# Kernel tuning notes

Measured on AMD Instinct MI355X. Metric: run time of the kernel, lower is better.

Reference implementation:

```python
import jax, jax.numpy as jnp
import numpy as np

N_NODES = 50000
N_EDGES = 600000
IN_DIM = 128
HID = 256
OUT = 3


def setup_inputs() -> dict:
    key = jax.random.key(0)
    ks = jax.random.split(key, 10)
    x = jax.random.normal(ks[0], (N_NODES, IN_DIM), dtype=jnp.float32)
    edge_index = jax.random.randint(ks[1], (2, N_EDGES), 0, N_NODES, dtype=jnp.int64)
    s = lambda k, shp: jax.random.normal(k, shp, dtype=jnp.float32) * (1.0 / np.sqrt(shp[0]))
    return {
        "x": x,
        "edge_index": edge_index,
        # SAGEConv1: lin_l (applied to aggregated neighbors, with bias), lin_r (root, no bias)
        "W1l": s(ks[2], (IN_DIM, HID)), "b1": jnp.zeros((HID,), jnp.float32), "W1r": s(ks[3], (IN_DIM, HID)),
        # SAGEConv2
        "W2l": s(ks[4], (HID, HID)), "b2": jnp.zeros((HID,), jnp.float32), "W2r": s(ks[5], (HID, HID)),
        # classification head
        "Wh": s(ks[6], (HID, OUT)), "bh": jnp.zeros((OUT,), jnp.float32),
    }


def _sage_conv(x, edge_index, Wl, b, Wr):
    """PyG SAGEConv with mean aggregation: out = lin_l(mean_{j->i} x_j) + lin_r(x_i)."""
    src, dst = edge_index[0], edge_index[1]
    n = x.shape[0]
    # gather source features and scatter-mean onto targets
    msg_sum = jax.ops.segment_sum(x[src], dst, num_segments=n)          # [N, d]
    deg = jax.ops.segment_sum(jnp.ones((src.shape[0],), x.dtype), dst, num_segments=n)
    mean = msg_sum / jnp.maximum(deg, 1.0)[:, None]                      # isolated nodes -> 0
    return mean @ Wl + b + x @ Wr


def reference(x, edge_index, W1l, b1, W1r, W2l, b2, W2r, Wh, bh):
    h = jax.nn.relu(_sage_conv(x, edge_index, W1l, b1, W1r))
    # dropout(p=0.2) is identity in eval mode
    h = jax.nn.relu(_sage_conv(h, edge_index, W2l, b2, W2r))
    return h @ Wh + bh
```

## Files before the change

kernel.cpp:

```cpp
#include <hip/hip_runtime.h>
#include <hip/hip_bf16.h>

#define N_NODES 50000
#define N_EDGES 600000
#define IN_DIM 128
#define HID 256
#define OUT_DIM 3

#define M_PAD 50048

#define SCAN_B 256
#define SCAN_NB ((N_NODES + SCAN_B - 1) / SCAN_B)

#define XQ_SCALE (255.0f / 12.0f)
#define XQ_INV   (12.0f / 255.0f)
#define XQ_OFF   (-6.0f)
#define HQ_SCALE (255.0f / 8.0f)
#define HQ_INV   (8.0f / 255.0f)

typedef __bf16 bf16x8 __attribute__((ext_vector_type(8)));
typedef float f32x4 __attribute__((ext_vector_type(4)));

static __device__ __forceinline__ unsigned short f2b(float f) {
    union { float f; unsigned u; } u; u.f = f;
    unsigned r = u.u + 0x7fffu + ((u.u >> 16) & 1u);
    return (unsigned short)(r >> 16);
}
static __device__ __forceinline__ float b2f(unsigned short b) {
    union { unsigned u; float f; } u; u.u = ((unsigned)b) << 16;
    return u.f;
}


#define SETUP_CAST (N_NODES * IN_DIM / 4)
#define SETUP_T1 (SETUP_CAST + 196608)
#define SETUP_T2 (SETUP_T1 + N_NODES * 3)
#define SETUP_TOT (SETUP_T2 + N_EDGES)

__global__ __launch_bounds__(256) void setup_kernel(
    const float* __restrict__ x, unsigned short* __restrict__ xb, unsigned* __restrict__ xq,
    const float* __restrict__ W1l, const float* __restrict__ W1r,
    const float* __restrict__ W2l, const float* __restrict__ W2r,
    unsigned short* __restrict__ W1lt, unsigned short* __restrict__ W1rt,
    unsigned short* __restrict__ W2lt, unsigned short* __restrict__ W2rt,
    const float* __restrict__ bh, float* __restrict__ out,
    const int* __restrict__ dst, int* __restrict__ counts) {
    int i = blockIdx.x * blockDim.x + threadIdx.x;
    if (i < SETUP_CAST) {
        float4 v = ((const float4*)x)[i];
        ushort4 o;
        o.x = f2b(v.x); o.y = f2b(v.y); o.z = f2b(v.z); o.w = f2b(v.w);
        ((ushort4*)xb)[i] = o;
        float t0 = fminf(fmaxf((v.x - XQ_OFF) * XQ_SCALE, 0.f), 255.f);
        float t1 = fminf(fmaxf((v.y - XQ_OFF) * XQ_SCALE, 0.f), 255.f);
        float t2 = fminf(fmaxf((v.z - XQ_OFF) * XQ_SCALE, 0.f), 255.f);
        float t3 = fminf(fmaxf((v.w - XQ_OFF) * XQ_SCALE, 0.f), 255.f);
        unsigned q = (unsigned)(t0 + 0.5f) | ((unsigned)(t1 + 0.5f) << 8) |
                     ((unsigned)(t2 + 0.5f) << 16) | ((unsigned)(t3 + 0.5f) << 24);
        xq[i] = q;
    } else if (i < SETUP_T1) {
        int j = i - SETUP_CAST;
        const float* in; unsigned short* ow; int K;
        if (j < 32768)       { in = W1l; ow = W1lt; K = IN_DIM; }
        else if (j < 65536)  { in = W1r; ow = W1rt; K = IN_DIM; j -= 32768; }
        else if (j < 131072) { in = W2l; ow = W2lt; K = HID;    j -= 65536; }
        else                 { in = W2r; ow = W2rt; K = HID;    j -= 131072; }
        int k = j >> 8;
        int n = j & 255;
        ow[(size_t)n * K + k] = f2b(in[j]);
    } else if (i < SETUP_T2) {
        int j = i - SETUP_T1;
        out[j] = bh[j % 3];
    } else if (i < SETUP_TOT) {
        int e = i - SETUP_T2;
        atomicAdd(&counts[dst[e]], 1);
    }
}


__global__ __launch_bounds__(256) void block_sum_kernel(const int* __restrict__ counts,
                                                        int* __restrict__ partial) {
    int node = blockIdx.x * SCAN_B + threadIdx.x;
    int v = (node < N_NODES) ? counts[node] : 0;
#pragma unroll
    for (int off = 32; off > 0; off >>= 1) v += __shfl_down(v, off);
    __shared__ int ws[4];
    if ((threadIdx.x & 63) == 0) ws[threadIdx.x >> 6] = v;
    __syncthreads();
    if (threadIdx.x == 0) partial[blockIdx.x] = ws[0] + ws[1] + ws[2] + ws[3];
}

__global__ __launch_bounds__(256) void scan_partial_kernel(int* __restrict__ partial) {
    __shared__ int s[SCAN_B];
    int t = threadIdx.x;
    int v = (t < SCAN_NB) ? partial[t] : 0;
    s[t] = v;
    __syncthreads();
    for (int off = 1; off < SCAN_B; off <<= 1) {
        int u = (t >= off) ? s[t - off] : 0;
        __syncthreads();
        s[t] += u;
        __syncthreads();
    }
    if (t < SCAN_NB) partial[t] = s[t] - v;
}

__global__ __launch_bounds__(256) void write_rowptr_kernel(const int* __restrict__ counts,
                                                           const int* __restrict__ partial,
                                                           int* __restrict__ row_ptr) {
    __shared__ int s[SCAN_B];
    int t = threadIdx.x;
    int node = blockIdx.x * SCAN_B + t;
    int v = (node < N_NODES) ? counts[node] : 0;
    s[t] = v;
    __syncthreads();
    for (int off = 1; off < SCAN_B; off <<= 1) {
        int u = (t >= off) ? s[t - off] : 0;
        __syncthreads();
        s[t] += u;
        __syncthreads();
    }
    if (node < N_NODES) row_ptr[node] = partial[blockIdx.x] + s[t] - v;
    if (node == 0) row_ptr[N_NODES] = N_EDGES;
}

__global__ void fill_csr_kernel(const int* __restrict__ src, const int* __restrict__ dst,
                                const int* __restrict__ row_ptr, int* __restrict__ cursor,
                                int* __restrict__ csr_src) {
    int e = blockIdx.x * blockDim.x + threadIdx.x;
    if (e < N_EDGES) {
        int d = dst[e];
        int pos = atomicAdd(&cursor[d], 1);
        csr_src[row_ptr[d] + pos] = src[e];
    }
}


__global__ __launch_bounds__(256) void cast_h1_u8_kernel(const unsigned short* __restrict__ h1,
                                                         unsigned char* __restrict__ h1q) {
    int i = blockIdx.x * blockDim.x + threadIdx.x;
    if (i >= N_NODES * HID / 8) return;
    uint4 v = ((const uint4*)h1)[i];
    unsigned w[4] = {v.x, v.y, v.z, v.w};
    unsigned b0 = 0, b1 = 0;
#pragma unroll
    for (int k = 0; k < 4; k++) {
        float f0 = b2f((unsigned short)(w[k] & 0xffff));
        float f1 = b2f((unsigned short)(w[k] >> 16));
        unsigned q0 = (unsigned)(fminf(f0 * HQ_SCALE, 255.f) + 0.5f);
        unsigned q1 = (unsigned)(fminf(f1 * HQ_SCALE, 255.f) + 0.5f);
        if (k < 2) b0 |= (q0 << (k * 16)) | (q1 << (k * 16 + 8));
        else       b1 |= (q0 << ((k - 2) * 16)) | (q1 << ((k - 2) * 16 + 8));
    }
    ((uint2*)h1q)[i] = make_uint2(b0, b1);
}


static __device__ __forceinline__ void addb(unsigned* acc, uint4 v) {
    acc[0]  += v.x & 0xff; acc[1]  += (v.x >> 8) & 0xff; acc[2]  += (v.x >> 16) & 0xff; acc[3]  += v.x >> 24;
    acc[4]  += v.y & 0xff; acc[5]  += (v.y >> 8) & 0xff; acc[6]  += (v.y >> 16) & 0xff; acc[7]  += v.y >> 24;
    acc[8]  += v.z & 0xff; acc[9]  += (v.z >> 8) & 0xff; acc[10] += (v.z >> 16) & 0xff; acc[11] += v.z >> 24;
    acc[12] += v.w & 0xff; acc[13] += (v.w >> 8) & 0xff; acc[14] += (v.w >> 16) & 0xff; acc[15] += v.w >> 24;
}

static __device__ __forceinline__ uint4 pack8(const float* a) {
    uint4 pk;
    pk.x = (unsigned)f2b(a[0]) | ((unsigned)f2b(a[1]) << 16);
    pk.y = (unsigned)f2b(a[2]) | ((unsigned)f2b(a[3]) << 16);
    pk.z = (unsigned)f2b(a[4]) | ((unsigned)f2b(a[5]) << 16);
    pk.w = (unsigned)f2b(a[6]) | ((unsigned)f2b(a[7]) << 16);
    return pk;
}

__global__ __launch_bounds__(256) void agg_mean256_u8_kernel(const unsigned char* __restrict__ featq,
                                                             const int* __restrict__ row_ptr,
                                                             const int* __restrict__ csr_src,
                                                             unsigned short* __restrict__ out) {
    int node = blockIdx.x * 4 + (threadIdx.x >> 6);
    if (node >= N_NODES) return;
    int lane = threadIdx.x & 63;
    int g = lane >> 4, lq = lane & 15;
    const uint4* f = (const uint4*)featq;
    unsigned acc[16];
#pragma unroll
    for (int j = 0; j < 16; j++) acc[j] = 0u;
    int beg = row_ptr[node], end = row_ptr[node + 1];
    int i = beg;
    for (; i + 16 <= end; i += 16) {
        int s0 = csr_src[i + g];
        int s1 = csr_src[i + 4 + g];
        int s2 = csr_src[i + 8 + g];
        int s3 = csr_src[i + 12 + g];
        uint4 v0 = f[(size_t)s0 * 16 + lq];
        uint4 v1 = f[(size_t)s1 * 16 + lq];
        uint4 v2 = f[(size_t)s2 * 16 + lq];
        uint4 v3 = f[(size_t)s3 * 16 + lq];
        addb(acc, v0); addb(acc, v1); addb(acc, v2); addb(acc, v3);
    }
    int r = end - i;
    int rem = r & 3;
    int tb = i + (r & ~3);
    bool tl = g < rem;
    uint4 u0, u1, u2, ut;
    if (r >= 4)  { int s = csr_src[i + g];     u0 = f[(size_t)s * 16 + lq]; }
    if (r >= 8)  { int s = csr_src[i + 4 + g]; u1 = f[(size_t)s * 16 + lq]; }
    if (r >= 12) { int s = csr_src[i + 8 + g]; u2 = f[(size_t)s * 16 + lq]; }
    if (tl)      { int s = csr_src[tb + g];    ut = f[(size_t)s * 16 + lq]; }
    if (r >= 4)  addb(acc, u0);
    if (r >= 8)  addb(acc, u1);
    if (r >= 12) addb(acc, u2);
    if (tl) addb(acc, ut);
#pragma unroll
    for (int j = 0; j < 16; j++) {
        acc[j] += (unsigned)__shfl_xor((int)acc[j], 32);
        acc[j] += (unsigned)__shfl_xor((int)acc[j], 16);
    }
    float inv = (end > beg) ? HQ_INV / (float)(end - beg) : 0.0f;
    if (g == 0) {
        float m[16];
#pragma unroll
        for (int j = 0; j < 16; j++) m[j] = (float)acc[j] * inv;
        uint4* orow = (uint4*)(out + (size_t)node * 256);
        orow[lq * 2]     = pack8(m);
        orow[lq * 2 + 1] = pack8(m + 8);
    }
}

__global__ __launch_bounds__(256) void agg_mean128_u8_kernel(const unsigned char* __restrict__ featq,
                                                             const int* __restrict__ row_ptr,
                                                             const int* __restrict__ csr_src,
                                                             unsigned short* __restrict__ out) {
    int node = blockIdx.x * 4 + (threadIdx.x >> 6);
    if (node >= N_NODES) return;
    int lane = threadIdx.x & 63;
    int g = lane >> 3, lq = lane & 7;
    const uint4* f = (const uint4*)featq;
    unsigned acc[16];
#pragma unroll
    for (int j = 0; j < 16; j++) acc[j] = 0u;
    int beg = row_ptr[node], end = row_ptr[node + 1];
    int i = beg;
    for (; i + 16 <= end; i += 16) {
        int s0 = csr_src[i + g];
        int s1 = csr_src[i + 8 + g];
        uint4 v0 = f[(size_t)s0 * 8 + lq];
        uint4 v1 = f[(size_t)s1 * 8 + lq];
        addb(acc, v0); addb(acc, v1);
    }
    int r = end - i;
    int rem = r & 7;
    int tb = i + (r & ~7);
    bool tl = g < rem;
    uint4 u0, ut;
    if (r >= 8) { int s = csr_src[i + g];  u0 = f[(size_t)s * 8 + lq]; }
    if (tl)     { int s = csr_src[tb + g]; ut = f[(size_t)s * 8 + lq]; }
    if (r >= 8) addb(acc, u0);
    if (tl) addb(acc, ut);
#pragma unroll
    for (int j = 0; j < 16; j++) {
        acc[j] += (unsigned)__shfl_xor((int)acc[j], 32);
        acc[j] += (unsigned)__shfl_xor((int)acc[j], 16);
        acc[j] += (unsigned)__shfl_xor((int)acc[j], 8);
    }
    bool has = end > beg;
    float inv = has ? XQ_INV / (float)(end - beg) : 0.0f;
    float o = has ? XQ_OFF : 0.0f;
    if (g == 0) {
        float m[16];
#pragma unroll
        for (int j = 0; j < 16; j++) m[j] = (float)acc[j] * inv + o;
        uint4* orow = (uint4*)(out + (size_t)node * 128);
        orow[lq * 2]     = pack8(m);
        orow[lq * 2 + 1] = pack8(m + 8);
    }
}


template <int KP>
static __device__ __forceinline__ void gemm_pipe_loop(
    const unsigned short* __restrict__ A0, const unsigned short* __restrict__ W0t,
    const unsigned short* __restrict__ A1, const unsigned short* __restrict__ W1t,
    unsigned short* As, unsigned short* Bs,
    int m0, int n0, int t, int w, int quad, int lr, f32x4 (&acc)[2][8]) {
    constexpr int KI = KP / 32;
    constexpr int NIT = 2 * KI;
    const int kb = t & 3;
    const int r  = t >> 2;

    const unsigned short* Aa[2] = {A0, A1};
    const unsigned short* Wa[2] = {W0t, W1t};

    uint4 ra0, ra1, rb0, rb1;
    auto gload = [&](int it) {
        int p = it / KI;
        int k0 = (it % KI) * 32 + kb * 8;
        const unsigned short* A = Aa[p];
        const unsigned short* Wt = Wa[p];
        ra0 = *(const uint4*)(A + (size_t)(m0 + r) * KP + k0);
        ra1 = *(const uint4*)(A + (size_t)(m0 + 64 + r) * KP + k0);
        rb0 = *(const uint4*)(Wt + (size_t)(n0 + r) * KP + k0);
        rb1 = *(const uint4*)(Wt + (size_t)(n0 + 64 + r) * KP + k0);
    };
    auto wlds = [&](int buf) {
        unsigned short* pa = As + buf * 4096;
        unsigned short* pb = Bs + buf * 4096;
        *(uint4*)&pa[(kb * 128 + r) * 8] = ra0;
        *(uint4*)&pa[(kb * 128 + 64 + r) * 8] = ra1;
        *(uint4*)&pb[(kb * 128 + r) * 8] = rb0;
        *(uint4*)&pb[(kb * 128 + 64 + r) * 8] = rb1;
    };

    gload(0);
    wlds(0);
    __syncthreads();
    for (int it = 0; it < NIT; ++it) {
        if (it + 1 < NIT) gload(it + 1);
        const unsigned short* pa = As + (it & 1) * 4096;
        const unsigned short* pb = Bs + (it & 1) * 4096;
        bf16x8 a[2], b[8];
        a[0] = *(const bf16x8*)&pa[(quad * 128 + w * 32 + lr) * 8];
        a[1] = *(const bf16x8*)&pa[(quad * 128 + w * 32 + 16 + lr) * 8];
#pragma unroll
        for (int nt = 0; nt < 8; nt++)
            b[nt] = *(const bf16x8*)&pb[(quad * 128 + nt * 16 + lr) * 8];
#pragma unroll
        for (int mt = 0; mt < 2; mt++)
#pragma unroll
            for (int nt = 0; nt < 8; nt++)
                acc[mt][nt] = __builtin_amdgcn_mfma_f32_16x16x32_bf16(a[mt], b[nt], acc[mt][nt], 0, 0, 0);
        if (it + 1 < NIT) {
            wlds((it + 1) & 1);
            __syncthreads();
        }
    }
}

template <int KP>
__global__ __launch_bounds__(256) void gemm_pipe_kernel(
    const unsigned short* __restrict__ A0, const unsigned short* __restrict__ W0t,
    const unsigned short* __restrict__ A1, const unsigned short* __restrict__ W1t,
    const float* __restrict__ bias, unsigned short* __restrict__ out, int M) {
    __shared__ __align__(16) unsigned short As[2 * 4096];
    __shared__ __align__(16) unsigned short Bs[2 * 4096];

    const int t = threadIdx.x;
    const int w = t >> 6, l = t & 63;
    const int quad = l >> 4, lr = l & 15;
    const int m0 = blockIdx.y * 128, n0 = blockIdx.x * 128;

    f32x4 acc[2][8];
    const f32x4 zero = {0.f, 0.f, 0.f, 0.f};
#pragma unroll
    for (int mt = 0; mt < 2; mt++)
#pragma unroll
        for (int nt = 0; nt < 8; nt++) acc[mt][nt] = zero;

    float bias_r[8];
#pragma unroll
    for (int nt = 0; nt < 8; nt++) bias_r[nt] = bias[n0 + nt * 16 + lr];

    gemm_pipe_loop<KP>(A0, W0t, A1, W1t, As, Bs, m0, n0, t, w, quad, lr, acc);

#pragma unroll
    for (int mt = 0; mt < 2; mt++)
#pragma unroll
        for (int r = 0; r < 4; r++) {
            int gm = m0 + w * 32 + mt * 16 + quad * 4 + r;
            if (gm >= M) continue;
            unsigned short* orow = out + (size_t)gm * HID;
#pragma unroll
            for (int nt = 0; nt < 8; nt++) {
                float v = fmaxf(acc[mt][nt][r] + bias_r[nt], 0.f);
                orow[n0 + nt * 16 + lr] = f2b(v);
            }
        }
}

template <int KP>
__global__ __launch_bounds__(256) void gemm_pipe_head_kernel(
    const unsigned short* __restrict__ A0, const unsigned short* __restrict__ W0t,
    const unsigned short* __restrict__ A1, const unsigned short* __restrict__ W1t,
    const float* __restrict__ bias, const float* __restrict__ Wh,
    float* __restrict__ out, int M) {
    __shared__ __align__(16) unsigned short As[2 * 4096];
    __shared__ __align__(16) unsigned short Bs[2 * 4096];

    const int t = threadIdx.x;
    const int w = t >> 6, l = t & 63;
    const int quad = l >> 4, lr = l & 15;
    const int m0 = blockIdx.y * 128, n0 = blockIdx.x * 128;

    f32x4 acc[2][8];
    const f32x4 zero = {0.f, 0.f, 0.f, 0.f};
#pragma unroll
    for (int mt = 0; mt < 2; mt++)
#pragma unroll
        for (int nt = 0; nt < 8; nt++) acc[mt][nt] = zero;

    float bias_r[8];
    float wh_r[8][3];
#pragma unroll
    for (int nt = 0; nt < 8; nt++) {
        int gn = n0 + nt * 16 + lr;
        bias_r[nt] = bias[gn];
        wh_r[nt][0] = Wh[gn * 3 + 0];
        wh_r[nt][1] = Wh[gn * 3 + 1];
        wh_r[nt][2] = Wh[gn * 3 + 2];
    }

    gemm_pipe_loop<KP>(A0, W0t, A1, W1t, As, Bs, m0, n0, t, w, quad, lr, acc);

#pragma unroll
    for (int mt = 0; mt < 2; mt++)
#pragma unroll
        for (int r = 0; r < 4; r++) {
            int gm = m0 + w * 32 + mt * 16 + quad * 4 + r;
            float p0 = 0.f, p1 = 0.f, p2 = 0.f;
#pragma unroll
            for (int nt = 0; nt < 8; nt++) {
                float v = fmaxf(acc[mt][nt][r] + bias_r[nt], 0.f);
                p0 += v * wh_r[nt][0];
                p1 += v * wh_r[nt][1];
                p2 += v * wh_r[nt][2];
            }
#pragma unroll
            for (int off = 1; off < 16; off <<= 1) {
                p0 += __shfl_xor(p0, off);
                p1 += __shfl_xor(p1, off);
                p2 += __shfl_xor(p2, off);
            }
            if (lr == 0 && gm < M) {
                atomicAdd(&out[(size_t)gm * 3 + 0], p0);
                atomicAdd(&out[(size_t)gm * 3 + 1], p1);
                atomicAdd(&out[(size_t)gm * 3 + 2], p2);
            }
        }
}


extern "C" void kernel_launch(void* const* d_in, const int* in_sizes, int n_in,
                              void* d_out, int out_size, void* d_ws, size_t ws_size,
                              hipStream_t stream) {
    const float* x   = (const float*)d_in[0];
    const int*   ei  = (const int*)d_in[1];
    const int*   src = ei;
    const int*   dst = ei + N_EDGES;
    const float* W1l = (const float*)d_in[2];
    const float* b1  = (const float*)d_in[3];
    const float* W1r = (const float*)d_in[4];
    const float* W2l = (const float*)d_in[5];
    const float* b2  = (const float*)d_in[6];
    const float* W2r = (const float*)d_in[7];
    const float* Wh  = (const float*)d_in[8];
    const float* bh  = (const float*)d_in[9];
    float* out = (float*)d_out;

    char* ws = (char*)d_ws;
    size_t off = 0;
    auto alloc = [&](size_t bytes) -> void* {
        void* p = ws + off;
        off = (off + bytes + 255) & ~(size_t)255;
        return p;
    };
    int* counts   = (int*)alloc((size_t)N_NODES * 4);
    int* row_ptr  = (int*)alloc((size_t)(N_NODES + 1) * 4);
    int* cursor   = (int*)alloc((size_t)N_NODES * 4);
    int* partial  = (int*)alloc((size_t)SCAN_NB * 4);
    int* csr_src  = (int*)alloc((size_t)N_EDGES * 4);
    unsigned short* xb   = (unsigned short*)alloc((size_t)M_PAD * IN_DIM * 2);
    unsigned short* agg  = (unsigned short*)alloc((size_t)M_PAD * HID * 2);
    unsigned short* h1   = (unsigned short*)alloc((size_t)M_PAD * HID * 2);
    unsigned short* W1lt = (unsigned short*)alloc((size_t)IN_DIM * HID * 2);
    unsigned short* W1rt = (unsigned short*)alloc((size_t)IN_DIM * HID * 2);
    unsigned short* W2lt = (unsigned short*)alloc((size_t)HID * HID * 2);
    unsigned short* W2rt = (unsigned short*)alloc((size_t)HID * HID * 2);
    unsigned*       xq   = (unsigned*)alloc((size_t)N_NODES * IN_DIM);
    unsigned char*  h1q  = (unsigned char*)alloc((size_t)N_NODES * HID);

    hipMemsetAsync(counts, 0, (size_t)N_NODES * 4, stream);
    hipMemsetAsync(cursor, 0, (size_t)N_NODES * 4, stream);

    setup_kernel<<<(SETUP_TOT + 255) / 256, 256, 0, stream>>>(
        x, xb, xq, W1l, W1r, W2l, W2r, W1lt, W1rt, W2lt, W2rt, bh, out, dst, counts);

    const int eblocks = (N_EDGES + 255) / 256;
    block_sum_kernel<<<SCAN_NB, SCAN_B, 0, stream>>>(counts, partial);
    scan_partial_kernel<<<1, SCAN_B, 0, stream>>>(partial);
    write_rowptr_kernel<<<SCAN_NB, SCAN_B, 0, stream>>>(counts, partial, row_ptr);
    fill_csr_kernel<<<eblocks, 256, 0, stream>>>(src, dst, row_ptr, cursor, csr_src);

    const int nblocks4 = (N_NODES + 3) / 4;
    dim3 gg(HID / 128, M_PAD / 128);

    agg_mean128_u8_kernel<<<nblocks4, 256, 0, stream>>>((const unsigned char*)xq, row_ptr, csr_src, agg);
    gemm_pipe_kernel<IN_DIM><<<gg, 256, 0, stream>>>(agg, W1lt, xb, W1rt, b1, h1, N_NODES);

    cast_h1_u8_kernel<<<(N_NODES * HID / 8 + 255) / 256, 256, 0, stream>>>(h1, h1q);

    agg_mean256_u8_kernel<<<nblocks4, 256, 0, stream>>>(h1q, row_ptr, csr_src, agg);
    gemm_pipe_head_kernel<HID><<<gg, 256, 0, stream>>>(agg, W2lt, h1, W2rt, b2, Wh, out, N_NODES);
}
```

Baseline: 283.8 us.

## Replace pipelined GEMMs with LDS-resident weight-panel GEMMs and fuse h1 quantization

Both SAGE GEMMs now load a full 64-column weight panel (both lin_l and lin_r halves) into swizzled LDS once per block. A operands are read directly from global memory into MFMA registers, which drops the double-buffered A/B staging and per-k-step barriers. The first GEMM also writes the uint8-quantized h1 in its epilogue, so the separate cast kernel and its extra pass over h1 are gone. The trade-offs are uncoalesced, unshared A loads straight from global, byte-granular h1q stores, and a larger LDS footprint (64 KB for the second GEMM) that limits occupancy.

After: 314.8 us. 1.11x slower.

```diff
diff --git a/kernel.cpp b/kernel.cpp
--- a/kernel.cpp
+++ b/kernel.cpp
@@ -136,26 +136,6 @@
 }
 
 
-__global__ __launch_bounds__(256) void cast_h1_u8_kernel(const unsigned short* __restrict__ h1,
-                                                         unsigned char* __restrict__ h1q) {
-    int i = blockIdx.x * blockDim.x + threadIdx.x;
-    if (i >= N_NODES * HID / 8) return;
-    uint4 v = ((const uint4*)h1)[i];
-    unsigned w[4] = {v.x, v.y, v.z, v.w};
-    unsigned b0 = 0, b1 = 0;
-#pragma unroll
-    for (int k = 0; k < 4; k++) {
-        float f0 = b2f((unsigned short)(w[k] & 0xffff));
-        float f1 = b2f((unsigned short)(w[k] >> 16));
-        unsigned q0 = (unsigned)(fminf(f0 * HQ_SCALE, 255.f) + 0.5f);
-        unsigned q1 = (unsigned)(fminf(f1 * HQ_SCALE, 255.f) + 0.5f);
-        if (k < 2) b0 |= (q0 << (k * 16)) | (q1 << (k * 16 + 8));
-        else       b1 |= (q0 << ((k - 2) * 16)) | (q1 << ((k - 2) * 16 + 8));
-    }
-    ((uint2*)h1q)[i] = make_uint2(b0, b1);
-}
-
-
 static __device__ __forceinline__ void addb(unsigned* acc, uint4 v) {
     acc[0]  += v.x & 0xff; acc[1]  += (v.x >> 8) & 0xff; acc[2]  += (v.x >> 16) & 0xff; acc[3]  += v.x >> 24;
     acc[4]  += v.y & 0xff; acc[5]  += (v.y >> 8) & 0xff; acc[6]  += (v.y >> 16) & 0xff; acc[7]  += v.y >> 24;
@@ -276,148 +256,160 @@
 }
 
 
-template <int KP>
-static __device__ __forceinline__ void gemm_pipe_loop(
-    const unsigned short* __restrict__ A0, const unsigned short* __restrict__ W0t,
-    const unsigned short* __restrict__ A1, const unsigned short* __restrict__ W1t,
-    unsigned short* As, unsigned short* Bs,
-    int m0, int n0, int t, int w, int quad, int lr, f32x4 (&acc)[2][8]) {
-    constexpr int KI = KP / 32;
-    constexpr int NIT = 2 * KI;
-    const int kb = t & 3;
-    const int r  = t >> 2;
-
-    const unsigned short* Aa[2] = {A0, A1};
-    const unsigned short* Wa[2] = {W0t, W1t};
-
-    uint4 ra0, ra1, rb0, rb1;
-    auto gload = [&](int it) {
-        int p = it / KI;
-        int k0 = (it % KI) * 32 + kb * 8;
-        const unsigned short* A = Aa[p];
-        const unsigned short* Wt = Wa[p];
-        ra0 = *(const uint4*)(A + (size_t)(m0 + r) * KP + k0);
-        ra1 = *(const uint4*)(A + (size_t)(m0 + 64 + r) * KP + k0);
-        rb0 = *(const uint4*)(Wt + (size_t)(n0 + r) * KP + k0);
-        rb1 = *(const uint4*)(Wt + (size_t)(n0 + 64 + r) * KP + k0);
-    };
-    auto wlds = [&](int buf) {
-        unsigned short* pa = As + buf * 4096;
-        unsigned short* pb = Bs + buf * 4096;
-        *(uint4*)&pa[(kb * 128 + r) * 8] = ra0;
-        *(uint4*)&pa[(kb * 128 + 64 + r) * 8] = ra1;
-        *(uint4*)&pb[(kb * 128 + r) * 8] = rb0;
-        *(uint4*)&pb[(kb * 128 + 64 + r) * 8] = rb1;
-    };
-
-    gload(0);
-    wlds(0);
+__global__ __launch_bounds__(256) void gemm1_bpanel_kernel(
+    const unsigned short* __restrict__ A0,
+    const unsigned short* __restrict__ A1,
+    const unsigned short* __restrict__ W0t,
+    const unsigned short* __restrict__ W1t,
+    const float* __restrict__ bias,
+    unsigned short* __restrict__ h1, unsigned char* __restrict__ h1q) {
+    __shared__ __align__(16) unsigned short Bs[64 * 256];
+    const int t = threadIdx.x;
+    const int nq = blockIdx.y;
+    {
+        int row = t & 63;
+        int gn = nq * 64 + row;
+        int cbase = (t >> 6) * 8;
+#pragma unroll
+        for (int j = 0; j < 8; ++j) {
+            int c = cbase + j;
+            uint4 v;
+            if (c < 16) v = *(const uint4*)(W0t + (size_t)gn * 128 + c * 8);
+            else        v = *(const uint4*)(W1t + (size_t)gn * 128 + (c - 16) * 8);
+            *(uint4*)&Bs[((size_t)row * 32 + (c ^ (row & 15))) * 8] = v;
+        }
+    }
     __syncthreads();
-    for (int it = 0; it < NIT; ++it) {
-        if (it + 1 < NIT) gload(it + 1);
-        const unsigned short* pa = As + (it & 1) * 4096;
-        const unsigned short* pb = Bs + (it & 1) * 4096;
-        bf16x8 a[2], b[8];
-        a[0] = *(const bf16x8*)&pa[(quad * 128 + w * 32 + lr) * 8];
-        a[1] = *(const bf16x8*)&pa[(quad * 128 + w * 32 + 16 + lr) * 8];
-#pragma unroll
-        for (int nt = 0; nt < 8; nt++)
-            b[nt] = *(const bf16x8*)&pb[(quad * 128 + nt * 16 + lr) * 8];
-#pragma unroll
-        for (int mt = 0; mt < 2; mt++)
-#pragma unroll
-            for (int nt = 0; nt < 8; nt++)
+
+    const int w = t >> 6, l = t & 63;
+    const int lr = l & 15, kh = l >> 4;
+    const int mbase = blockIdx.x * 256 + w * 64;
+    if (mbase >= M_PAD) return;
+
+    f32x4 acc[4][4];
+    const f32x4 zero = {0.f, 0.f, 0.f, 0.f};
+#pragma unroll
+    for (int mt = 0; mt < 4; mt++)
+#pragma unroll
+        for (int nt = 0; nt < 4; nt++) acc[mt][nt] = zero;
+
+#pragma unroll
+    for (int ks = 0; ks < 8; ++ks) {
+        const unsigned short* Ap = (ks < 4) ? A0 : A1;
+        int kk = (ks & 3) * 32 + kh * 8;
+        bf16x8 a[4], b[4];
+#pragma unroll
+        for (int mt = 0; mt < 4; mt++)
+            a[mt] = *(const bf16x8*)(Ap + (size_t)(mbase + mt * 16 + lr) * 128 + kk);
+#pragma unroll
+        for (int nt = 0; nt < 4; nt++) {
+            int row = nt * 16 + lr;
+            int c = (ks * 4 + kh) ^ lr;
+            b[nt] = *(const bf16x8*)&Bs[((size_t)row * 32 + c) * 8];
+        }
+#pragma unroll
+        for (int mt = 0; mt < 4; mt++)
+#pragma unroll
+            for (int nt = 0; nt < 4; nt++)
                 acc[mt][nt] = __builtin_amdgcn_mfma_f32_16x16x32_bf16(a[mt], b[nt], acc[mt][nt], 0, 0, 0);
-        if (it + 1 < NIT) {
-            wlds((it + 1) & 1);
-            __syncthreads();
-        }
-    }
-}
-
-template <int KP>
-__global__ __launch_bounds__(256) void gemm_pipe_kernel(
-    const unsigned short* __restrict__ A0, const unsigned short* __restrict__ W0t,
-    const unsigned short* __restrict__ A1, const unsigned short* __restrict__ W1t,
-    const float* __restrict__ bias, unsigned short* __restrict__ out, int M) {
-    __shared__ __align__(16) unsigned short As[2 * 4096];
-    __shared__ __align__(16) unsigned short Bs[2 * 4096];
-
+    }
+
+    float bias_r[4];
+#pragma unroll
+    for (int nt = 0; nt < 4; nt++) bias_r[nt] = bias[nq * 64 + nt * 16 + lr];
+#pragma unroll
+    for (int mt = 0; mt < 4; mt++)
+#pragma unroll
+        for (int r = 0; r < 4; r++) {
+            int gm = mbase + mt * 16 + kh * 4 + r;
+            if (gm >= N_NODES) continue;
+#pragma unroll
+            for (int nt = 0; nt < 4; nt++) {
+                int col = nq * 64 + nt * 16 + lr;
+                float v = fmaxf(acc[mt][nt][r] + bias_r[nt], 0.f);
+                h1[(size_t)gm * 256 + col] = f2b(v);
+                h1q[(size_t)gm * 256 + col] = (unsigned char)(fminf(v * HQ_SCALE, 255.f) + 0.5f);
+            }
+        }
+}
+
+__global__ __launch_bounds__(512) void gemm2_bpanel_head_kernel(
+    const unsigned short* __restrict__ A0,
+    const unsigned short* __restrict__ A1,
+    const unsigned short* __restrict__ W0t,
+    const unsigned short* __restrict__ W1t,
+    const float* __restrict__ bias, const float* __restrict__ Wh,
+    float* __restrict__ out) {
+    __shared__ __align__(16) unsigned short Bs[64 * 512];
     const int t = threadIdx.x;
+    const int nq = blockIdx.y;
+    {
+        int row = t & 63;
+        int gn = nq * 64 + row;
+        int cbase = (t >> 6) * 8;
+#pragma unroll
+        for (int j = 0; j < 8; ++j) {
+            int c = cbase + j;
+            uint4 v;
+            if (c < 32) v = *(const uint4*)(W0t + (size_t)gn * 256 + c * 8);
+            else        v = *(const uint4*)(W1t + (size_t)gn * 256 + (c - 32) * 8);
+            *(uint4*)&Bs[((size_t)row * 64 + (c ^ (row & 15))) * 8] = v;
+        }
+    }
+    __syncthreads();
+
     const int w = t >> 6, l = t & 63;
-    const int quad = l >> 4, lr = l & 15;
-    const int m0 = blockIdx.y * 128, n0 = blockIdx.x * 128;
-
-    f32x4 acc[2][8];
+    const int lr = l & 15, kh = l >> 4;
+    const int mbase = blockIdx.x * 512 + w * 64;
+    if (mbase >= M_PAD) return;
+
+    f32x4 acc[4][4];
     const f32x4 zero = {0.f, 0.f, 0.f, 0.f};
 #pragma unroll
-    for (int mt = 0; mt < 2; mt++)
-#pragma unroll
-        for (int nt = 0; nt < 8; nt++) acc[mt][nt] = zero;
-
-    float bias_r[8];
-#pragma unroll
-    for (int nt = 0; nt < 8; nt++) bias_r[nt] = bias[n0 + nt * 16 + lr];
-
-    gemm_pipe_loop<KP>(A0, W0t, A1, W1t, As, Bs, m0, n0, t, w, quad, lr, acc);
-
-#pragma unroll
-    for (int mt = 0; mt < 2; mt++)
-#pragma unroll
-        for (int r = 0; r < 4; r++) {
-            int gm = m0 + w * 32 + mt * 16 + quad * 4 + r;
-            if (gm >= M) continue;
-            unsigned short* orow = out + (size_t)gm * HID;
-#pragma unroll
-            for (int nt = 0; nt < 8; nt++) {
-                float v = fmaxf(acc[mt][nt][r] + bias_r[nt], 0.f);
-                orow[n0 + nt * 16 + lr] = f2b(v);
-            }
-        }
-}
-
-template <int KP>
-__global__ __launch_bounds__(256) void gemm_pipe_head_kernel(
-    const unsigned short* __restrict__ A0, const unsigned short* __restrict__ W0t,
-    const unsigned short* __restrict__ A1, const unsigned short* __restrict__ W1t,
-    const float* __restrict__ bias, const float* __restrict__ Wh,
-    float* __restrict__ out, int M) {
-    __shared__ __align__(16) unsigned short As[2 * 4096];
-    __shared__ __align__(16) unsigned short Bs[2 * 4096];
-
-    const int t = threadIdx.x;
-    const int w = t >> 6, l = t & 63;
-    const int quad = l >> 4, lr = l & 15;
-    const int m0 = blockIdx.y * 128, n0 = blockIdx.x * 128;
-
-    f32x4 acc[2][8];
-    const f32x4 zero = {0.f, 0.f, 0.f, 0.f};
-#pragma unroll
-    for (int mt = 0; mt < 2; mt++)
-#pragma unroll
-        for (int nt = 0; nt < 8; nt++) acc[mt][nt] = zero;
-
-    float bias_r[8];
-    float wh_r[8][3];
-#pragma unroll
-    for (int nt = 0; nt < 8; nt++) {
-        int gn = n0 + nt * 16 + lr;
+    for (int mt = 0; mt < 4; mt++)
+#pragma unroll
+        for (int nt = 0; nt < 4; nt++) acc[mt][nt] = zero;
+
+#pragma unroll
+    for (int ks = 0; ks < 16; ++ks) {
+        const unsigned short* Ap = (ks < 8) ? A0 : A1;
+        int kk = (ks & 7) * 32 + kh * 8;
+        bf16x8 a[4], b[4];
+#pragma unroll
+        for (int mt = 0; mt < 4; mt++)
+            a[mt] = *(const bf16x8*)(Ap + (size_t)(mbase + mt * 16 + lr) * 256 + kk);
+#pragma unroll
+        for (int nt = 0; nt < 4; nt++) {
+            int row = nt * 16 + lr;
+            int c = (ks * 4 + kh) ^ lr;
+            b[nt] = *(const bf16x8*)&Bs[((size_t)row * 64 + c) * 8];
+        }
+#pragma unroll
+        for (int mt = 0; mt < 4; mt++)
+#pragma unroll
+            for (int nt = 0; nt < 4; nt++)
+                acc[mt][nt] = __builtin_amdgcn_mfma_f32_16x16x32_bf16(a[mt], b[nt], acc[mt][nt], 0, 0, 0);
+    }
+
+    float bias_r[4];
+    float wh_r[4][3];
+#pragma unroll
+    for (int nt = 0; nt < 4; nt++) {
+        int gn = nq * 64 + nt * 16 + lr;
         bias_r[nt] = bias[gn];
         wh_r[nt][0] = Wh[gn * 3 + 0];
         wh_r[nt][1] = Wh[gn * 3 + 1];
         wh_r[nt][2] = Wh[gn * 3 + 2];
     }
 
-    gemm_pipe_loop<KP>(A0, W0t, A1, W1t, As, Bs, m0, n0, t, w, quad, lr, acc);
-
-#pragma unroll
-    for (int mt = 0; mt < 2; mt++)
+#pragma unroll
+    for (int mt = 0; mt < 4; mt++)
 #pragma unroll
         for (int r = 0; r < 4; r++) {
-            int gm = m0 + w * 32 + mt * 16 + quad * 4 + r;
+            int gm = mbase + mt * 16 + kh * 4 + r;
             float p0 = 0.f, p1 = 0.f, p2 = 0.f;
 #pragma unroll
-            for (int nt = 0; nt < 8; nt++) {
+            for (int nt = 0; nt < 4; nt++) {
                 float v = fmaxf(acc[mt][nt][r] + bias_r[nt], 0.f);
                 p0 += v * wh_r[nt][0];
                 p1 += v * wh_r[nt][1];
@@ -429,7 +421,7 @@
                 p1 += __shfl_xor(p1, off);
                 p2 += __shfl_xor(p2, off);
             }
-            if (lr == 0 && gm < M) {
+            if (lr == 0 && gm < N_NODES) {
                 atomicAdd(&out[(size_t)gm * 3 + 0], p0);
                 atomicAdd(&out[(size_t)gm * 3 + 1], p1);
                 atomicAdd(&out[(size_t)gm * 3 + 2], p2);
@@ -475,7 +467,7 @@
     unsigned short* W2lt = (unsigned short*)alloc((size_t)HID * HID * 2);
     unsigned short* W2rt = (unsigned short*)alloc((size_t)HID * HID * 2);
     unsigned*       xq   = (unsigned*)alloc((size_t)N_NODES * IN_DIM);
-    unsigned char*  h1q  = (unsigned char*)alloc((size_t)N_NODES * HID);
+    unsigned char*  h1q  = (unsigned char*)alloc((size_t)M_PAD * HID);
 
     hipMemsetAsync(counts, 0, (size_t)N_NODES * 4, stream);
     hipMemsetAsync(cursor, 0, (size_t)N_NODES * 4, stream);
@@ -490,13 +482,10 @@
     fill_csr_kernel<<<eblocks, 256, 0, stream>>>(src, dst, row_ptr, cursor, csr_src);
 
     const int nblocks4 = (N_NODES + 3) / 4;
-    dim3 gg(HID / 128, M_PAD / 128);
 
     agg_mean128_u8_kernel<<<nblocks4, 256, 0, stream>>>((const unsigned char*)xq, row_ptr, csr_src, agg);
-    gemm_pipe_kernel<IN_DIM><<<gg, 256, 0, stream>>>(agg, W1lt, xb, W1rt, b1, h1, N_NODES);
-
-    cast_h1_u8_kernel<<<(N_NODES * HID / 8 + 255) / 256, 256, 0, stream>>>(h1, h1q);
+    gemm1_bpanel_kernel<<<dim3(196, 4), 256, 0, stream>>>(agg, xb, W1lt, W1rt, b1, h1, h1q);
 
     agg_mean256_u8_kernel<<<nblocks4, 256, 0, stream>>>(h1q, row_ptr, csr_src, agg);
-    gemm_pipe_head_kernel<HID><<<gg, 256, 0, stream>>>(agg, W2lt, h1, W2rt, b2, Wh, out, N_NODES);
-}
+    gemm2_bpanel_head_kernel<<<dim3(98, 4), 512, 0, stream>>>(agg, h1, W2lt, W2rt, b2, Wh, out);
+}
```
